# Kernel tuning notes

Hardware: AMD Instinct MI355X
Metric: run time of the kernel (lower is better)

Reference implementation:

```python
import jax, jax.numpy as jnp
import numpy as np

N, E, G = 30000, 240000, 1500
EMB, NODE_DIM, EDGE_DIM, TASKS = 300, 9, 3, 12
L_ENC, L_RAT = 5, 2
GAMMA, T_CON = 0.4, 0.2


def _w(key, shape, fan_in):
    return jax.random.normal(key, shape, jnp.float32) / np.float32(np.sqrt(fan_in))


def setup_inputs() -> dict:
    key = jax.random.key(0)
    ks = jax.random.split(key, 32)
    inp = {}
    inp['x'] = jax.random.normal(ks[0], (N, NODE_DIM), jnp.float32)
    inp['edge_attr'] = jax.random.normal(ks[1], (E, EDGE_DIM), jnp.float32)
    inp['edge_index'] = jax.random.randint(ks[2], (2, E), 0, N, jnp.int32)
    b = jnp.sort(jax.random.randint(ks[3], (N,), 0, G, jnp.int32))
    inp['batch'] = b.at[0].set(0).at[-1].set(G - 1)
    u = jax.random.uniform(ks[4], (N, 2), jnp.float32, 1e-6, 1.0 - 1e-6)
    inp['gumbel'] = -jnp.log(-jnp.log(u))  # standard Gumbel noise (tau=1)
    inp['perm'] = jax.random.permutation(ks[5], G).astype(jnp.int32)
    inp['W_enc'] = _w(ks[6], (NODE_DIM, EMB), NODE_DIM)
    inp['b_enc'] = jnp.zeros((EMB,), jnp.float32)
    inp['We_g'] = _w(ks[7], (L_ENC, EDGE_DIM, EMB), EDGE_DIM)
    inp['be_g'] = jnp.zeros((L_ENC, EMB), jnp.float32)
    inp['W1_g'] = _w(ks[8], (L_ENC, EMB, 2 * EMB), EMB)
    inp['b1_g'] = jnp.zeros((L_ENC, 2 * EMB), jnp.float32)
    inp['W2_g'] = _w(ks[9], (L_ENC, 2 * EMB, EMB), 2 * EMB)
    inp['b2_g'] = jnp.zeros((L_ENC, EMB), jnp.float32)
    inp['We_r'] = _w(ks[10], (L_RAT, EDGE_DIM, EMB), EDGE_DIM)
    inp['be_r'] = jnp.zeros((L_RAT, EMB), jnp.float32)
    inp['W1_r'] = _w(ks[11], (L_RAT, EMB, 2 * EMB), EMB)
    inp['b1_r'] = jnp.zeros((L_RAT, 2 * EMB), jnp.float32)
    inp['W2_r'] = _w(ks[12], (L_RAT, 2 * EMB, EMB), 2 * EMB)
    inp['b2_r'] = jnp.zeros((L_RAT, EMB), jnp.float32)
    inp['Wg1'] = _w(ks[13], (EMB, 2 * EMB), EMB)
    inp['bg1'] = jnp.zeros((2 * EMB,), jnp.float32)
    inp['Wg2'] = _w(ks[14], (2 * EMB, 2), 2 * EMB)
    inp['bg2'] = jnp.zeros((2,), jnp.float32)
    inp['Wp1'] = _w(ks[15], (EMB, 2 * EMB), EMB)
    inp['bp1'] = jnp.zeros((2 * EMB,), jnp.float32)
    inp['Wp2'] = _w(ks[16], (2 * EMB, TASKS), 2 * EMB)
    inp['bp2'] = jnp.zeros((TASKS,), jnp.float32)
    return inp


def _gin_stack(x, src, dst, edge_attr, We, be, W1, b1, W2, b2):
    # GIN-style message passing with edge features, residual, JK='last'.
    L = We.shape[0]
    for l in range(L):
        e = edge_attr @ We[l] + be[l]                               # [E, EMB]
        msg = jax.nn.relu(x[src] + e)                                # gather [E, EMB]
        agg = jax.ops.segment_sum(msg, dst, num_segments=x.shape[0])  # scatter [N, EMB]
        h = jax.nn.relu((agg + x) @ W1[l] + b1[l]) @ W2[l] + b2[l]
        if l < L - 1:
            h = jax.nn.relu(h)
        x = x + h  # residual
    return x


def _mlp2(h, Wa, ba, Wb, bb):
    # Linear -> (BN=identity in eval) -> ReLU -> (Dropout=identity) -> Linear
    return jax.nn.relu(h @ Wa + ba) @ Wb + bb


def _forward(x, edge_attr, gumbel, W_enc, b_enc, We_g, be_g, W1_g, b1_g, W2_g, b2_g,
             We_r, be_r, W1_r, b1_r, W2_r, b2_r, Wg1, bg1, Wg2, bg2, Wp1, bp1, Wp2, bp2,
             edge_index, batch, perm):
    src, dst = edge_index[0], edge_index[1]
    cnt = jnp.clip(jax.ops.segment_sum(jnp.ones((x.shape[0],), jnp.float32), batch, num_segments=G), 1.0)[:, None]

    def gmean(v):
        return jax.ops.segment_sum(v, batch, num_segments=G) / cnt

    x_feat = x @ W_enc + b_enc                                      # node encoder
    h_node = _gin_stack(x_feat, src, dst, edge_attr, We_g, be_g, W1_g, b1_g, W2_g, b2_g)
    x_rat = _gin_stack(x_feat, src, dst, edge_attr, We_r, be_r, W1_r, b1_r, W2_r, b2_r)

    gate_logits = _mlp2(x_rat, Wg1, bg1, Wg2, bg2)                  # [N, 2]
    gate = jax.nn.softmax(gate_logits + gumbel, axis=-1)[:, 1:2]     # gumbel-softmax (soft), keep last col

    h_r = gmean(gate * h_node)
    h_env = gmean((1.0 - gate) * h_node)
    r_num = jax.ops.segment_sum(gate, batch, num_segments=G) + 1e-8
    env_num = jax.ops.segment_sum(1.0 - gate, batch, num_segments=G) + 1e-8

    pred_rem = _mlp2(h_r, Wp1, bp1, Wp2, bp2)
    loss_reg = jnp.abs(r_num / (r_num + env_num) - GAMMA).mean()

    h_out = gmean(h_node)
    na = jnp.linalg.norm(h_r, axis=1)
    nb = jnp.linalg.norm(h_out, axis=1)
    nc = jnp.linalg.norm(h_env, axis=1)
    sim = jnp.exp((h_r @ h_out.T) / (na[:, None] * nb[None, :] + 1e-8) / T_CON)
    sim_cp = jnp.exp((h_r @ h_env.T) / (na[:, None] * nc[None, :] + 1e-8) / T_CON)
    pos = jnp.diagonal(sim)
    loss_con = -jnp.log(pos / (sim_cp.sum(axis=1) + pos)).mean()

    pred_rep = _mlp2(h_r + h_env[perm], Wp1, bp1, Wp2, bp2)
    return pred_rep, pred_rem, loss_reg, loss_con


def reference(x, edge_attr, gumbel, W_enc, b_enc, We_g, be_g, W1_g, b1_g, W2_g, b2_g,
              We_r, be_r, W1_r, b1_r, W2_r, b2_r, Wg1, bg1, Wg2, bg2, Wp1, bp1, Wp2, bp2,
              edge_index, batch, perm):
    return _forward(x, edge_attr, gumbel, W_enc, b_enc, We_g, be_g, W1_g, b1_g, W2_g, b2_g,
                    We_r, be_r, W1_r, b1_r, W2_r, b2_r, Wg1, bg1, Wg2, bg2, Wp1, bp1, Wp2, bp2,
                    edge_index, batch, perm)
```

## Files before the change

kernel.cpp:

```cpp
#include <hip/hip_runtime.h>
#include <hip/hip_bf16.h>

typedef __hip_bfloat16 bf16;
typedef __attribute__((ext_vector_type(8))) short bf16x8;
typedef __attribute__((ext_vector_type(4))) float f32x4;

#define NN 30000
#define NE 240000
#define NG 1500
#define EMB 300
#define HID 600
#define NTASK 12
#define SEM 320
#define SHID 608
#define CG 75
#define NBLK_SCAN 118

__device__ __forceinline__ float tof(bf16 v){ return __bfloat162float(v); }
__device__ __forceinline__ bf16  tob(float v){ return __float2bfloat16(v); }
__device__ __forceinline__ float b2f(unsigned short u){ return __uint_as_float(((unsigned)u)<<16); }

__global__ __launch_bounds__(256) void k_hist(const int* __restrict__ dst, int* __restrict__ deg){
    int e = blockIdx.x*256 + threadIdx.x;
    if (e < NE) atomicAdd(&deg[dst[e]], 1);
// ... 37 lines not shown
        __syncthreads();
        s[t] += add;
        __syncthreads();
    }
    int excl = s[t] - v + boff[b];
    if (i < NN){ indptr[i] = excl; cursor[i] = excl; }
    if (i == 0) indptr[NN] = NE;
}

__global__ __launch_bounds__(256) void k_scatter(const int* __restrict__ dst, int* __restrict__ cursor,
                                                 int* __restrict__ eid){
    int e = blockIdx.x*256 + threadIdx.x;
    if (e < NE){ int p = atomicAdd(&cursor[dst[e]], 1); eid[p] = e; }
}

__global__ __launch_bounds__(256) void k_eprep(const int* __restrict__ eid, const int* __restrict__ src,
                                               const float* __restrict__ eattr, float4* __restrict__ epack){
    int k = blockIdx.x*256 + threadIdx.x;
    if (k >= NE) return;
    int e = eid[k];
    float4 p;
    p.x = __int_as_float(src[e]);
    p.y = eattr[e*3]; p.z = eattr[e*3+1]; p.w = eattr[e*3+2];
    epack[k] = p;
}

__global__ __launch_bounds__(256) void k_wprep_all(
        const float* __restrict__ W1_g, const float* __restrict__ W2_g,
        const float* __restrict__ W1_r, const float* __restrict__ W2_r,
        const float* __restrict__ Wg1,  const float* __restrict__ Wp1,
        bf16* __restrict__ wt1g, bf16* __restrict__ wt2g,
        bf16* __restrict__ wt1r, bf16* __restrict__ wt2r,
        bf16* __restrict__ wtg1, bf16* __restrict__ wtp1,
        int* __restrict__ deg, const int* __restrict__ batch, int* __restrict__ gstart){
    __shared__ float t[32][33];
    int z = blockIdx.z;
    if (z == 16){
        int i = (blockIdx.y*19 + blockIdx.x)*256 + threadIdx.x;
        if (i < NN) deg[i] = 0;
        return;
    }
    if (z == 17){
        int g = (blockIdx.y*19 + blockIdx.x)*256 + threadIdx.x;
        if (g > NG) return;
        if (g == NG){ gstart[NG] = NN; return; }
        int lo=0, hi=NN;
        while (lo<hi){ int mid=(lo+hi)>>1; if (batch[mid] < g) lo=mid+1; else hi=mid; }
        gstart[g] = lo;
        return;
    }
    const float* Ws; bf16* Wd; int K, Kp, N;
    if (z < 5)      { Ws = W1_g + (size_t)z*EMB*HID;      Wd = wt1g + (size_t)z*HID*SEM;      K=EMB; Kp=SEM;  N=HID; }
    else if (z < 10){ int l=z-5;  Ws = W2_g + (size_t)l*HID*EMB; Wd = wt2g + (size_t)l*EMB*SHID; K=HID; Kp=SHID; N=EMB; }
    else if (z < 12){ int l=z-10; Ws = W1_r + (size_t)l*EMB*HID; Wd = wt1r + (size_t)l*HID*SEM;  K=EMB; Kp=SEM;  N=HID; }
    else if (z < 14){ int l=z-12; Ws = W2_r + (size_t)l*HID*EMB; Wd = wt2r + (size_t)l*EMB*SHID; K=HID; Kp=SHID; N=EMB; }
    else if (z ==14){ Ws = Wg1; Wd = wtg1; K=EMB; Kp=SEM; N=HID; }
    else            { Ws = Wp1; Wd = wtp1; K=EMB; Kp=SEM; N=HID; }
    int n0 = blockIdx.x*32, k0 = blockIdx.y*32;
    if (n0 >= N || k0 >= Kp) return;
    int tx = threadIdx.x & 31, ty = threadIdx.x >> 5;
    #pragma unroll
    for (int i=0;i<4;i++){
        int k = k0 + ty + i*8, n = n0 + tx;
        t[ty+i*8][tx] = (k<K && n<N) ? Ws[(size_t)k*N+n] : 0.f;
    }
    __syncthreads();
    #pragma unroll
    for (int i=0;i<4;i++){
        int n = n0 + ty + i*8, k = k0 + tx;
        if (n<N && k<Kp) Wd[(size_t)n*Kp+k] = tob(t[tx][ty+i*8]);
    }
}

__global__ __launch_bounds__(256) void k_encoder(const float* __restrict__ x, const float* __restrict__ W,
                                                 const float* __restrict__ b, bf16* __restrict__ xfeat){
    int idx = blockIdx.x*256 + threadIdx.x;
    if (idx >= NN*EMB) return;
    int n = idx / EMB, c = idx - n*EMB;
    float acc = b[c];
    #pragma unroll
    for (int k=0;k<9;k++) acc += x[n*9+k] * W[k*EMB+c];
    xfeat[(size_t)n*SEM + c] = tob(acc);
}

__device__ __forceinline__ void agg4_body(const bf16* __restrict__ cur, const float* __restrict__ We,
                      const float* __restrict__ be, const float4* __restrict__ epack,
                      const int* __restrict__ indptr, bf16* __restrict__ apx, int idx){
    int n = idx / CG, cg = idx - n*CG;
    int c0 = cg*4;
    float w0[4], w1[4], w2[4], bbv[4], acc[4];
    #pragma unroll
    for (int j=0;j<4;j++){
        w0[j] = We[c0+j]; w1[j] = We[EMB+c0+j]; w2[j] = We[2*EMB+c0+j]; bbv[j] = be[c0+j];
    }
    ushort4 hs = *(const ushort4*)&cur[(size_t)n*SEM + c0];
    acc[0]=b2f(hs.x); acc[1]=b2f(hs.y); acc[2]=b2f(hs.z); acc[3]=b2f(hs.w);
    int k  = indptr[n], k1 = indptr[n+1];

    auto accum4 = [&](float4 e0, float4 e1, float4 e2, float4 e3,
                      ushort4 ha, ushort4 hb, ushort4 hc, ushort4 hd){
        float fa[4] = {b2f(ha.x), b2f(ha.y), b2f(ha.z), b2f(ha.w)};
        float fb[4] = {b2f(hb.x), b2f(hb.y), b2f(hb.z), b2f(hb.w)};
        float fc[4] = {b2f(hc.x), b2f(hc.y), b2f(hc.z), b2f(hc.w)};
        float fd[4] = {b2f(hd.x), b2f(hd.y), b2f(hd.z), b2f(hd.w)};
        #pragma unroll
        for (int j=0;j<4;j++){
            float va = fa[j] + e0.y*w0[j] + e0.z*w1[j] + e0.w*w2[j] + bbv[j];
            float vb = fb[j] + e1.y*w0[j] + e1.z*w1[j] + e1.w*w2[j] + bbv[j];
            float vc = fc[j] + e2.y*w0[j] + e2.z*w1[j] + e2.w*w2[j] + bbv[j];
            float vd = fd[j] + e3.y*w0[j] + e3.z*w1[j] + e3.w*w2[j] + bbv[j];
            acc[j] += fmaxf(va, 0.f) + fmaxf(vb, 0.f) + fmaxf(vc, 0.f) + fmaxf(vd, 0.f);
        }
    };

    if (k + 4 <= k1){
// ... 82 lines not shown
        ushort4 hb = *(const ushort4*)&cur[(size_t)s1*SEM + c0];
        float fa[4] = {b2f(ha.x), b2f(ha.y), b2f(ha.z), b2f(ha.w)};
        float fb[4] = {b2f(hb.x), b2f(hb.y), b2f(hb.z), b2f(hb.w)};
        #pragma unroll
        for (int j=0;j<4;j++){
            accA[j] += fmaxf(fa[j] + e0.y*a0[j] + e0.z*a1[j] + e0.w*a2[j] + ab[j], 0.f)
                     + fmaxf(fb[j] + e1.y*a0[j] + e1.z*a1[j] + e1.w*a2[j] + ab[j], 0.f);
            accB[j] += fmaxf(fa[j] + e0.y*b0[j] + e0.z*b1[j] + e0.w*b2[j] + bb[j], 0.f)
                     + fmaxf(fb[j] + e1.y*b0[j] + e1.z*b1[j] + e1.w*b2[j] + bb[j], 0.f);
        }
    }
    if (k < k1){
        float4 e0 = epack[k];
        int s0 = __float_as_int(e0.x);
        ushort4 ha = *(const ushort4*)&cur[(size_t)s0*SEM + c0];
        float fa[4] = {b2f(ha.x), b2f(ha.y), b2f(ha.z), b2f(ha.w)};
        #pragma unroll
        for (int j=0;j<4;j++){
            accA[j] += fmaxf(fa[j] + e0.y*a0[j] + e0.z*a1[j] + e0.w*a2[j] + ab[j], 0.f);
            accB[j] += fmaxf(fa[j] + e0.y*b0[j] + e0.z*b1[j] + e0.w*b2[j] + bb[j], 0.f);
        }
    }
    ushort4 oA, oB;
    oA.x=__bfloat16_as_ushort(tob(accA[0])); oA.y=__bfloat16_as_ushort(tob(accA[1]));
    oA.z=__bfloat16_as_ushort(tob(accA[2])); oA.w=__bfloat16_as_ushort(tob(accA[3]));
    oB.x=__bfloat16_as_ushort(tob(accB[0])); oB.y=__bfloat16_as_ushort(tob(accB[1]));
    oB.z=__bfloat16_as_ushort(tob(accB[2])); oB.w=__bfloat16_as_ushort(tob(accB[3]));
    *(ushort4*)&apxA[(size_t)n*SEM + c0] = oA;
    *(ushort4*)&apxB[(size_t)n*SEM + c0] = oB;
}

__device__ __forceinline__ void gemm_body(const bf16* __restrict__ A, const bf16* __restrict__ Bt,
        const float* __restrict__ bias, const bf16* __restrict__ R, bf16* __restrict__ C,
        int M, int N, int Kp, int ldc, int relu_out, short* lds){
    short* Ct = lds;
    const int CS = 136;
    int tid = threadIdx.x;
    int wave = tid >> 6, lane = tid & 63;
    int wm = wave >> 1, wn = wave & 1;
    int m0 = blockIdx.y*128, n0 = blockIdx.x*128;

    int srow = tid >> 1;
    int sq   = (tid & 1) * 2;
    int grA = min(m0 + srow, M-1);
    int grB = min(n0 + srow, N-1);
    const bf16* pA = A  + (size_t)grA*Kp + sq*8;
    const bf16* pB = Bt + (size_t)grB*Kp + sq*8;
    int aoff0 = ((srow>>4)*64 +  sq   *16 + (srow&15))*8;
    int aoff1 = ((srow>>4)*64 + (sq+1)*16 + (srow&15))*8;

    f32x4 acc[4][4];
    #pragma unroll
    for (int i=0;i<4;i++){
        #pragma unroll
        for (int j=0;j<4;j++) acc[i][j] = (f32x4){0.f,0.f,0.f,0.f};
    }

    int KC = Kp >> 5;
    uint4 ra0 = *(const uint4*)(pA);
    uint4 ra1 = *(const uint4*)(pA + 8);
    uint4 rb0 = *(const uint4*)(pB);
    uint4 rb1 = *(const uint4*)(pB + 8);
    *(uint4*)(lds + aoff0)        = ra0;
    *(uint4*)(lds + aoff1)        = ra1;
    *(uint4*)(lds + 4096 + aoff0) = rb0;
    *(uint4*)(lds + 4096 + aoff1) = rb1;
    __syncthreads();
    if (KC > 1){
        ra0 = *(const uint4*)(pA + 32); ra1 = *(const uint4*)(pA + 40);
        rb0 = *(const uint4*)(pB + 32); rb1 = *(const uint4*)(pB + 40);
    }

    for (int kc=0; kc<KC; ++kc){
// ... 37 lines not shown
            for (int r=0;r<4;r++){
                float v = acc[i][j][r] + bv;
                if (relu_out) v = fmaxf(v, 0.f);
                Ct[(rl+r)*CS + cl] = (short)__bfloat16_as_ushort(tob(v));
            }
        }
    }
    __syncthreads();
    #pragma unroll
    for (int p=0;p<8;p++){
        int rl = p*16 + (tid>>4);
        int cl = (tid&15)*8;
        int row = m0 + rl, col = n0 + cl;
        if (row < M && col < N){
            union { short s8[8]; uint4 v; } u;
            u.v = *(uint4*)&Ct[rl*CS + cl];
            if (R){
                const bf16* rp = &R[(size_t)row*ldc + col];
                #pragma unroll
                for (int e=0;e<8;e++){
                    float v = b2f((unsigned short)u.s8[e]) + tof(rp[e]);
                    u.s8[e] = (short)__bfloat16_as_ushort(tob(v));
                }
            }
            *(uint4*)&C[(size_t)row*ldc + col] = u.v;
        }
    }
}

__global__ __launch_bounds__(256) void k_gemm2(const bf16* __restrict__ A, const bf16* __restrict__ Bt,
        const float* __restrict__ bias, const bf16* __restrict__ R, bf16* __restrict__ C,
        int M, int N, int Kp, int ldc, int relu_out){
    __shared__ __align__(16) char ldsbuf[34816];
    gemm_body(A, Bt, bias, R, C, M, N, Kp, ldc, relu_out, (short*)ldsbuf);
}

__global__ __launch_bounds__(256) void k_gemm2z(
        const bf16* __restrict__ A0, const bf16* __restrict__ A1,
        const bf16* __restrict__ Bt0, const bf16* __restrict__ Bt1,
        const float* __restrict__ bias0, const float* __restrict__ bias1,
        const bf16* __restrict__ R0, const bf16* __restrict__ R1,
        bf16* __restrict__ C0, bf16* __restrict__ C1,
        int M, int N, int Kp, int ldc, int relu0, int relu1){
    __shared__ __align__(16) char ldsbuf[34816];
    if (blockIdx.z == 0) gemm_body(A0, Bt0, bias0, R0, C0, M, N, Kp, ldc, relu0, (short*)ldsbuf);
    else                 gemm_body(A1, Bt1, bias1, R1, C1, M, N, Kp, ldc, relu1, (short*)ldsbuf);
}

__device__ __forceinline__ void stage_tile(const short* __restrict__ P, int RB, int K, int r0, int k0,
                                           short (*lds)[64][8], int tid){
    #pragma unroll
    for (int s=0;s<2;s++){
        int seg = tid*2+s;
        int row = seg>>2, q = seg&3;
        int gr = r0 + row;
        int gk = k0 + q*8;
        union { short s8[8]; uint4 v; } u;
        if (gr < RB && gk + 8 <= K){
            const uint2* p = (const uint2*)(P + (size_t)gr*K + gk);
            uint2 lo = p[0], hi = p[1];
            u.v.x = lo.x; u.v.y = lo.y; u.v.z = hi.x; u.v.w = hi.y;
        } else {
            #pragma unroll
            for (int j=0;j<8;j++){
                int kk = gk + j;
                u.s8[j] = (gr < RB && kk < K) ? P[(size_t)gr*K + kk] : (short)0;
            }
        }
        *(uint4*)&lds[row>>4][q*16 + (row&15)][0] = u.v;
    }
}

__device__ __forceinline__ void sim_body(const bf16* __restrict__ A, const bf16* __restrict__ Bt,
                      const float* __restrict__ na, const float* __restrict__ nc, float* __restrict__ C,
                      char* ldsraw){
    short (*Asl)[64][8] = (short(*)[64][8])ldsraw;
    short (*Bsl)[64][8] = (short(*)[64][8])(ldsraw + 8192);
    int tid = threadIdx.x;
    int wave = tid >> 6, lane = tid & 63;
    int wm = wave >> 1, wn = wave & 1;
    int m0 = blockIdx.y*128, n0 = blockIdx.x*128;
    f32x4 acc[4][4];
    #pragma unroll
    for (int i=0;i<4;i++){
        #pragma unroll
        for (int j=0;j<4;j++) acc[i][j] = (f32x4){0.f,0.f,0.f,0.f};
    }
    for (int k0=0; k0<SEM; k0+=32){
        stage_tile((const short*)A,  NG, SEM, m0, k0, Asl, tid);
        stage_tile((const short*)Bt, NG, SEM, n0, k0, Bsl, tid);
        __syncthreads();
        bf16x8 af[4], bfr[4];
        #pragma unroll
        for (int i=0;i<4;i++) af[i]  = *(const bf16x8*)&Asl[wm*4+i][lane][0];
        #pragma unroll
        for (int j=0;j<4;j++) bfr[j] = *(const bf16x8*)&Bsl[wn*4+j][lane][0];
        #pragma unroll
        for (int i=0;i<4;i++){
            #pragma unroll
            for (int j=0;j<4;j++)
                acc[i][j] = __builtin_amdgcn_mfma_f32_16x16x32_bf16(af[i], bfr[j], acc[i][j], 0, 0, 0);
        }
        __syncthreads();
    }
    int lq = lane >> 4, lr = lane & 15;
    #pragma unroll
    for (int i=0;i<4;i++){
        int rb = m0 + (wm*4+i)*16 + lq*4;
        #pragma unroll
        for (int j=0;j<4;j++){
            int col = n0 + (wn*4+j)*16 + lr;
            if (col >= NG) continue;
            float ncj = nc[col];
            #pragma unroll
            for (int r=0;r<4;r++){
                int row = rb + r;
                if (row >= NG) continue;
                C[(size_t)row*NG+col] = expf(acc[i][j][r] * 5.0f / (na[row]*ncj + 1e-8f));
            }
        }
    }
}

__global__ __launch_bounds__(256) void k_simhead(const bf16* __restrict__ hrb, const bf16* __restrict__ henvb,
        const float* __restrict__ na, const float* __restrict__ nc, float* __restrict__ simcp,
        const bf16* __restrict__ Pbuf, const bf16* __restrict__ wtp1, const float* __restrict__ bp1,
        bf16* __restrict__ hidP){
    __shared__ __align__(16) char ldsbuf[34816];
    if (blockIdx.z == 0){
        if (blockIdx.x >= 12 || blockIdx.y >= 12) return;
        sim_body(hrb, henvb, na, nc, simcp, ldsbuf);
    } else {
        if (blockIdx.x >= 5) return;
        gemm_body(Pbuf, wtp1, bp1, nullptr, hidP, 2*NG, HID, SEM, SHID, 1, (short*)ldsbuf);
    }
}

__global__ __launch_bounds__(256) void k_gate(const bf16* __restrict__ mid, const float* __restrict__ Wg2,
                      const float* __restrict__ bg2, const float* __restrict__ gumbel, float* __restrict__ gate){
    int gw = blockIdx.x*4 + (threadIdx.x >> 6);
    int lane = threadIdx.x & 63;
    if (gw >= NN) return;
    float s0=0.f, s1=0.f;
    for (int i=lane;i<HID;i+=64){
        float h = tof(mid[(size_t)gw*SHID+i]);
        s0 += h * Wg2[i*2];
        s1 += h * Wg2[i*2+1];
    }
    for (int off=32; off>0; off>>=1){ s0 += __shfl_down(s0, off); s1 += __shfl_down(s1, off); }
    if (lane==0){
        float l0 = s0 + bg2[0] + gumbel[gw*2];
        float l1 = s1 + bg2[1] + gumbel[gw*2+1];
        float m = fmaxf(l0,l1);
        float e0 = expf(l0-m), e1 = expf(l1-m);
        gate[gw] = e1/(e0+e1);
    }
}

__global__ __launch_bounds__(320) void k_pool(const bf16* __restrict__ h, const float* __restrict__ gate,
                      const int* __restrict__ gstart, float* __restrict__ sumh, float* __restrict__ sumgh,
                      float* __restrict__ rnum, float* __restrict__ cntf){
    int g = blockIdx.x, c = threadIdx.x;
    if (c >= EMB) return;
    int n0 = gstart[g], n1 = gstart[g+1];
    float sh=0.f, sg=0.f, sgate=0.f;
    for (int n=n0;n<n1;n++){
        float v = tof(h[(size_t)n*SEM+c]);
        float gt = gate[n];
        sh += v; sg += gt*v;
        if (c==0) sgate += gt;
    }
    sumh[g*EMB+c] = sh; sumgh[g*EMB+c] = sg;
    if (c==0){ rnum[g] = sgate; cntf[g] = (float)(n1-n0); }
}

__global__ __launch_bounds__(320) void k_meannorm(const float* __restrict__ sumh, const float* __restrict__ sumgh,
                      const float* __restrict__ cntf, float* __restrict__ hr, float* __restrict__ henv,
                      float* __restrict__ hout, bf16* __restrict__ hrb, bf16* __restrict__ henvb,
                      bf16* __restrict__ P, float* __restrict__ na, float* __restrict__ nc,
                      float* __restrict__ pos){
    int g = blockIdx.x, c = threadIdx.x;
    float r=0.f, e=0.f, o=0.f;
    int idx = g*SEM + c;
    if (c < EMB){
        int off = g*EMB + c;
        float inv = 1.f / fmaxf(cntf[g], 1.f);
        float sh = sumh[off], sg = sumgh[off];
        r = sg*inv; e = (sh-sg)*inv; o = sh*inv;
        hr[off] = r; henv[off] = e; hout[off] = o;
        hrb[idx] = tob(r); henvb[idx] = tob(e); P[idx] = tob(r);
    } else {
        hrb[idx] = tob(0.f); henvb[idx] = tob(0.f); P[idx] = tob(0.f);
    }
    float srr=r*r, soo=o*o, see=e*e, sro=r*o;
    #pragma unroll
    for (int off=32; off>0; off>>=1){
        srr += __shfl_down(srr,off); soo += __shfl_down(soo,off);
        see += __shfl_down(see,off); sro += __shfl_down(sro,off);
    }
    __shared__ float ws[4][5];
    int wv = c >> 6, ln = c & 63;
    if (ln == 0){ ws[0][wv]=srr; ws[1][wv]=soo; ws[2][wv]=see; ws[3][wv]=sro; }
    __syncthreads();
    if (c == 0){
        float a=0.f,b=0.f,c2=0.f,d=0.f;
        #pragma unroll
        for (int i=0;i<5;i++){ a+=ws[0][i]; b+=ws[1][i]; c2+=ws[2][i]; d+=ws[3][i]; }
        float sa = sqrtf(a), sb = sqrtf(b), sc = sqrtf(c2);
        na[g] = sa; nc[g] = sc;
        pos[g] = expf(d/(sa*sb + 1e-8f) * 5.0f);
    }
}

__global__ __launch_bounds__(256) void k_pbuild2(const float* __restrict__ hr, const float* __restrict__ henv,
                      const int* __restrict__ perm, bf16* __restrict__ P){
    int idx = blockIdx.x*256 + threadIdx.x;
    if (idx >= NG*SEM) return;
    int g = idx / SEM, c = idx - g*SEM;
    P[(size_t)(NG+g)*SEM + c] = (c < EMB)
        ? tob(hr[g*EMB+c] + henv[(size_t)perm[g]*EMB + c])
        : tob(0.f);
}

__global__ __launch_bounds__(256) void k_rowsum(const float* __restrict__ simcp, float* __restrict__ S){
    __shared__ float red[256];
    int g = blockIdx.x, t = threadIdx.x;
    float s = 0.f;
    for (int j=t;j<NG;j+=256) s += simcp[(size_t)g*NG+j];
    red[t]=s; __syncthreads();
    for (int off=128; off>0; off>>=1){ if (t<off) red[t]+=red[t+off]; __syncthreads(); }
    if (t==0) S[g]=red[0];
}

__global__ __launch_bounds__(256) void k_pred(const bf16* __restrict__ hidP, const float* __restrict__ Wp2,
                      const float* __restrict__ bp2, float* __restrict__ out){
    int r = blockIdx.x*4 + (threadIdx.x >> 6);
    int lane = threadIdx.x & 63;
    if (r >= 2*NG) return;
    float acc[NTASK];
    #pragma unroll
    for (int t=0;t<NTASK;t++) acc[t] = 0.f;
    for (int i=lane;i<HID;i+=64){
        float h = tof(hidP[(size_t)r*SHID+i]);
        const float4* wp = (const float4*)&Wp2[i*NTASK];
        float4 wa = wp[0], wb = wp[1], wc = wp[2];
        acc[0]+=h*wa.x; acc[1]+=h*wa.y; acc[2]+=h*wa.z; acc[3]+=h*wa.w;
        acc[4]+=h*wb.x; acc[5]+=h*wb.y; acc[6]+=h*wb.z; acc[7]+=h*wb.w;
        acc[8]+=h*wc.x; acc[9]+=h*wc.y; acc[10]+=h*wc.z; acc[11]+=h*wc.w;
    }
    #pragma unroll
    for (int t=0;t<NTASK;t++){
        for (int off=32; off>0; off>>=1) acc[t] += __shfl_down(acc[t], off);
    }
    if (lane==0){
        float* dst = (r < NG) ? &out[NG*NTASK + r*NTASK] : &out[(r-NG)*NTASK];
        #pragma unroll
        for (int t=0;t<NTASK;t++) dst[t] = acc[t] + bp2[t];
    }
}

__global__ __launch_bounds__(256) void k_loss(const float* __restrict__ cntf, const float* __restrict__ rnum,
                      const float* __restrict__ pos, const float* __restrict__ S, float* __restrict__ out){
    __shared__ float ra[256], rb[256];
    int t = threadIdx.x;
// ... 29 lines not shown
    const float* W1_g   = (const float*)d_in[10];
    const float* b1_g   = (const float*)d_in[11];
    const float* W2_g   = (const float*)d_in[12];
    const float* b2_g   = (const float*)d_in[13];
    const float* We_r   = (const float*)d_in[14];
    const float* be_r   = (const float*)d_in[15];
    const float* W1_r   = (const float*)d_in[16];
    const float* b1_r   = (const float*)d_in[17];
    const float* W2_r   = (const float*)d_in[18];
    const float* b2_r   = (const float*)d_in[19];
    const float* Wg1    = (const float*)d_in[20];
    const float* bg1    = (const float*)d_in[21];
    const float* Wg2    = (const float*)d_in[22];
    const float* bg2    = (const float*)d_in[23];
    const float* Wp1    = (const float*)d_in[24];
    const float* bp1    = (const float*)d_in[25];
    const float* Wp2    = (const float*)d_in[26];
    const float* bp2    = (const float*)d_in[27];
    float* out = (float*)d_out;

    const int* srcArr = eidx;
    const int* dstArr = eidx + NE;

    char* w = (char*)d_ws;
    size_t off = 0;
    auto alloc = [&](size_t bytes)->char*{ char* p = w + off; off += (bytes + 255) & ~(size_t)255; return p; };
    bf16* xfeat = (bf16*)alloc((size_t)NN*SEM*2);
    bf16* cur_r = (bf16*)alloc((size_t)NN*SEM*2);
    bf16* cur_g = (bf16*)alloc((size_t)NN*SEM*2);
    bf16* apx   = (bf16*)alloc((size_t)NN*SEM*2);
    bf16* apx2  = (bf16*)alloc((size_t)NN*SEM*2);
    char* midc  = alloc((size_t)NN*SHID*2);
    bf16* mid_r = (bf16*)midc;
    float* simcp = (float*)midc;
    bf16* Pbuf   = (bf16*)(midc + 12*1024*1024);
    bf16* hidP   = (bf16*)(midc + 20*1024*1024);
    bf16* mid_g = (bf16*)alloc((size_t)NN*SHID*2);
    bf16* wt1g  = (bf16*)alloc((size_t)5*HID*SEM*2);
    bf16* wt2g  = (bf16*)alloc((size_t)5*EMB*SHID*2);
    bf16* wt1r  = (bf16*)alloc((size_t)2*HID*SEM*2);
    bf16* wt2r  = (bf16*)alloc((size_t)2*EMB*SHID*2);
    bf16* wtg1  = (bf16*)alloc((size_t)HID*SEM*2);
    bf16* wtp1  = (bf16*)alloc((size_t)HID*SEM*2);
    float4* epack = (float4*)alloc((size_t)NE*16);
    float* gate  = (float*)alloc((size_t)NN*4);
    float* sumh  = (float*)alloc((size_t)NG*EMB*4);
    float* sumgh = (float*)alloc((size_t)NG*EMB*4);
    float* hr    = (float*)alloc((size_t)NG*EMB*4);
    float* henv  = (float*)alloc((size_t)NG*EMB*4);
    float* hout  = (float*)alloc((size_t)NG*EMB*4);
    bf16* hrb    = (bf16*)alloc((size_t)NG*SEM*2);
    bf16* henvb  = (bf16*)alloc((size_t)NG*SEM*2);
    float* rnum  = (float*)alloc(NG*4);
    float* cntf  = (float*)alloc(NG*4);
    float* na    = (float*)alloc(NG*4);
    float* ncv   = (float*)alloc(NG*4);
    float* pos   = (float*)alloc(NG*4);
    float* Ssum  = (float*)alloc(NG*4);
    int* deg     = (int*)alloc((size_t)NN*4);
    int* indptr  = (int*)alloc((size_t)(NN+1)*4);
    int* cursor  = (int*)alloc((size_t)NN*4);
    int* eid     = (int*)alloc((size_t)NE*4);
    int* gstart  = (int*)alloc((size_t)(NG+1)*4);
    int* bsum    = (int*)alloc((size_t)NBLK_SCAN*4);
    int* boff    = (int*)alloc((size_t)NBLK_SCAN*4);

    const int NB_NE  = (NE+255)/256;
    const int NB_NC  = (NN*EMB+255)/256;
    const int NB_AG  = (NN*CG+255)/256;
    const int NB_GP  = (NG*SEM+255)/256;

    dim3 gwp(19, 19, 18);
    k_wprep_all<<<gwp, 256, 0, stream>>>(W1_g, W2_g, W1_r, W2_r, Wg1, Wp1,
                                         wt1g, wt2g, wt1r, wt2r, wtg1, wtp1,
                                         deg, batch, gstart);

    k_hist   <<<NB_NE, 256, 0, stream>>>(dstArr, deg);
    k_scanA  <<<NBLK_SCAN, 256, 0, stream>>>(deg, bsum);
    k_scanB  <<<1, 128, 0, stream>>>(bsum, boff);
    k_scanC  <<<NBLK_SCAN, 256, 0, stream>>>(deg, boff, indptr, cursor);
    k_scatter<<<NB_NE, 256, 0, stream>>>(dstArr, cursor, eid);
    k_eprep  <<<NB_NE, 256, 0, stream>>>(eid, srcArr, eattr, epack);

    dim3 gm1z((HID+127)/128, (NN+127)/128, 2);
    dim3 gm2z((EMB+127)/128, (NN+127)/128, 2);
    dim3 gm1((HID+127)/128, (NN+127)/128);
    dim3 gm2((EMB+127)/128, (NN+127)/128);
    dim3 gagz(NB_AG, 1, 2);

    k_encoder<<<NB_NC, 256, 0, stream>>>(x, W_enc, b_enc, xfeat);

    k_agg4d<<<NB_AG, 256, 0, stream>>>(xfeat, We_r, be_r, We_g, be_g, epack, indptr, apx, apx2);
    k_gemm2z<<<gm1z, 256, 0, stream>>>(apx, apx2, wt1r, wt1g, b1_r, b1_g,
                                       nullptr, nullptr, mid_r, mid_g, NN, HID, SEM, SHID, 1, 1);
    k_gemm2z<<<gm2z, 256, 0, stream>>>(mid_r, mid_g, wt2r, wt2g, b2_r, b2_g,
                                       xfeat, xfeat, cur_r, cur_g, NN, EMB, SHID, SEM, 1, 1);

    k_agg4z<<<gagz, 256, 0, stream>>>(cur_r, cur_g, We_r + 3*EMB, We_g + 3*EMB, be_r + EMB, be_g + EMB,
                                      epack, indptr, apx, apx2);
    k_gemm2z<<<gm1z, 256, 0, stream>>>(apx, apx2, wt1r + (size_t)HID*SEM, wt1g + (size_t)HID*SEM,
                                       b1_r + HID, b1_g + HID, nullptr, nullptr, mid_r, mid_g,
                                       NN, HID, SEM, SHID, 1, 1);
    k_gemm2z<<<gm2z, 256, 0, stream>>>(mid_r, mid_g, wt2r + (size_t)EMB*SHID, wt2g + (size_t)EMB*SHID,
                                       b2_r + EMB, b2_g + EMB, cur_r, cur_g, cur_r, cur_g,
                                       NN, EMB, SHID, SEM, 0, 1);

    k_agg4 <<<NB_AG, 256, 0, stream>>>(cur_g, We_g + 2*3*EMB, be_g + 2*EMB, epack, indptr, apx2);
    k_gemm2z<<<gm1z, 256, 0, stream>>>(cur_r, apx2, wtg1, wt1g + (size_t)2*HID*SEM,
                                       bg1, b1_g + 2*HID, nullptr, nullptr, mid_r, mid_g,
                                       NN, HID, SEM, SHID, 1, 1);
    k_gemm2<<<gm2, 256, 0, stream>>>(mid_g, wt2g + (size_t)2*EMB*SHID, b2_g + 2*EMB, cur_g, cur_g,
                                     NN, EMB, SHID, SEM, 1);
    k_gate<<<NN/4, 256, 0, stream>>>(mid_r, Wg2, bg2, gumbel, gate);

    for (int l=3; l<5; l++){
        k_agg4 <<<NB_AG, 256, 0, stream>>>(cur_g, We_g + l*3*EMB, be_g + l*EMB, epack, indptr, apx2);
        k_gemm2<<<gm1, 256, 0, stream>>>(apx2, wt1g + (size_t)l*HID*SEM, b1_g + l*HID, nullptr, mid_g,
                                         NN, HID, SEM, SHID, 1);
        k_gemm2<<<gm2, 256, 0, stream>>>(mid_g, wt2g + (size_t)l*EMB*SHID, b2_g + l*EMB, cur_g, cur_g,
                                         NN, EMB, SHID, SEM, (l<4)?1:0);
    }

    k_pool    <<<NG, 320, 0, stream>>>(cur_g, gate, gstart, sumh, sumgh, rnum, cntf);
    k_meannorm<<<NG, 320, 0, stream>>>(sumh, sumgh, cntf, hr, henv, hout, hrb, henvb, Pbuf, na, ncv, pos);
    k_pbuild2 <<<NB_GP, 256, 0, stream>>>(hr, henv, perm, Pbuf);
    dim3 gsh(12, 24, 2);
    k_simhead<<<gsh, 256, 0, stream>>>(hrb, henvb, na, ncv, simcp, Pbuf, wtp1, bp1, hidP);
    k_rowsum<<<NG, 256, 0, stream>>>(simcp, Ssum);
    k_pred  <<<(2*NG+3)/4, 256, 0, stream>>>(hidP, Wp2, bp2, out);
    k_loss  <<<1, 256, 0, stream>>>(cntf, rnum, pos, Ssum, out);
}
```

Baseline: 963.0 us.

## Fuse gate head into GEMM epilogue, use 128x64 tiles, fold encoder and rowsum

Several changes land together. The encoder is folded into the weight-prep launch, and the gate's second layer is computed inside the first gate GEMM epilogue using shuffle reductions and atomics, so the mid_r activations are no longer re-read. The gate GEMM is also co-scheduled with the GNN layer's first GEMM in a single launch. The N=300 GEMMs switch to 128x64 tiles to cut padded-column waste, and the similarity row sums are reduced in the sim kernel's epilogue instead of writing a 1500x1500 matrix and summing it in a separate pass. The cost is float atomics, which make summation order nondeterministic, and extra zero-initialisation.

Result: slower. 1.005 ms (+4.3%).

```diff
diff --git a/kernel.cpp b/kernel.cpp
--- a/kernel.cpp
+++ b/kernel.cpp
@@ -93,12 +93,25 @@
         bf16* __restrict__ wt1g, bf16* __restrict__ wt2g,
         bf16* __restrict__ wt1r, bf16* __restrict__ wt2r,
         bf16* __restrict__ wtg1, bf16* __restrict__ wtp1,
-        int* __restrict__ deg, const int* __restrict__ batch, int* __restrict__ gstart){
+        int* __restrict__ deg, const int* __restrict__ batch, int* __restrict__ gstart,
+        const float* __restrict__ x, const float* __restrict__ W_enc,
+        const float* __restrict__ b_enc, bf16* __restrict__ xfeat,
+        float* __restrict__ glogit){
     __shared__ float t[32][33];
     int z = blockIdx.z;
+    if (z >= 18){
+        int idx = ((z-18)*361 + blockIdx.y*19 + blockIdx.x)*256 + threadIdx.x;
+        if (idx >= NN*EMB) return;
+        int n = idx / EMB, c = idx - n*EMB;
+        float acc = b_enc[c];
+        #pragma unroll
+        for (int k=0;k<9;k++) acc += x[n*9+k] * W_enc[k*EMB+c];
+        xfeat[(size_t)n*SEM + c] = tob(acc);
+        return;
+    }
     if (z == 16){
         int i = (blockIdx.y*19 + blockIdx.x)*256 + threadIdx.x;
-        if (i < NN) deg[i] = 0;
+        if (i < NN){ deg[i] = 0; glogit[2*i] = 0.f; glogit[2*i+1] = 0.f; }
         return;
     }
     if (z == 17){
@@ -131,17 +144,6 @@
         int n = n0 + ty + i*8, k = k0 + tx;
         if (n<N && k<Kp) Wd[(size_t)n*Kp+k] = tob(t[tx][ty+i*8]);
     }
-}
-
-__global__ __launch_bounds__(256) void k_encoder(const float* __restrict__ x, const float* __restrict__ W,
-                                                 const float* __restrict__ b, bf16* __restrict__ xfeat){
-    int idx = blockIdx.x*256 + threadIdx.x;
-    if (idx >= NN*EMB) return;
-    int n = idx / EMB, c = idx - n*EMB;
-    float acc = b[c];
-    #pragma unroll
-    for (int k=0;k<9;k++) acc += x[n*9+k] * W[k*EMB+c];
-    xfeat[(size_t)n*SEM + c] = tob(acc);
 }
 
 __device__ __forceinline__ void agg4_body(const bf16* __restrict__ cur, const float* __restrict__ We,
@@ -290,13 +292,12 @@
 
 __device__ __forceinline__ void gemm_body(const bf16* __restrict__ A, const bf16* __restrict__ Bt,
         const float* __restrict__ bias, const bf16* __restrict__ R, bf16* __restrict__ C,
-        int M, int N, int Kp, int ldc, int relu_out, short* lds){
+        int M, int N, int Kp, int ldc, int relu_out, short* lds, int m0, int n0){
     short* Ct = lds;
     const int CS = 136;
     int tid = threadIdx.x;
     int wave = tid >> 6, lane = tid & 63;
     int wm = wave >> 1, wn = wave & 1;
-    int m0 = blockIdx.y*128, n0 = blockIdx.x*128;
 
     int srow = tid >> 1;
     int sq   = (tid & 1) * 2;
@@ -400,7 +401,8 @@
         const float* __restrict__ bias, const bf16* __restrict__ R, bf16* __restrict__ C,
         int M, int N, int Kp, int ldc, int relu_out){
     __shared__ __align__(16) char ldsbuf[34816];
-    gemm_body(A, Bt, bias, R, C, M, N, Kp, ldc, relu_out, (short*)ldsbuf);
+    gemm_body(A, Bt, bias, R, C, M, N, Kp, ldc, relu_out, (short*)ldsbuf,
+              blockIdx.y*128, blockIdx.x*128);
 }
 
 __global__ __launch_bounds__(256) void k_gemm2z(
@@ -411,8 +413,256 @@
         bf16* __restrict__ C0, bf16* __restrict__ C1,
         int M, int N, int Kp, int ldc, int relu0, int relu1){
     __shared__ __align__(16) char ldsbuf[34816];
-    if (blockIdx.z == 0) gemm_body(A0, Bt0, bias0, R0, C0, M, N, Kp, ldc, relu0, (short*)ldsbuf);
-    else                 gemm_body(A1, Bt1, bias1, R1, C1, M, N, Kp, ldc, relu1, (short*)ldsbuf);
+    int m0 = blockIdx.y*128, n0 = blockIdx.x*128;
+    if (blockIdx.z == 0) gemm_body(A0, Bt0, bias0, R0, C0, M, N, Kp, ldc, relu0, (short*)ldsbuf, m0, n0);
+    else                 gemm_body(A1, Bt1, bias1, R1, C1, M, N, Kp, ldc, relu1, (short*)ldsbuf, m0, n0);
+}
+
+__device__ __forceinline__ void gemm64_body(const bf16* __restrict__ A, const bf16* __restrict__ Bt,
+        const float* __restrict__ bias, const bf16* __restrict__ R, bf16* __restrict__ C,
+        int M, int N, int Kp, int ldc, int relu_out, short* lds, int m0, int n0){
+    short* Ct = lds;
+    const int CS = 72;
+    int tid = threadIdx.x;
+    int wave = tid >> 6, lane = tid & 63;
+    int wm = wave >> 1, wn = wave & 1;
+
+    int srow = tid >> 1;
+    int sq   = (tid & 1) * 2;
+    int grA = min(m0 + srow, M-1);
+    const bf16* pA = A + (size_t)grA*Kp + sq*8;
+    int aoff0 = ((srow>>4)*64 +  sq   *16 + (srow&15))*8;
+    int aoff1 = ((srow>>4)*64 + (sq+1)*16 + (srow&15))*8;
+
+    int brow = tid >> 2;
+    int bq   = tid & 3;
+    int grB = min(n0 + brow, N-1);
+    const bf16* pB = Bt + (size_t)grB*Kp + bq*8;
+    int boff = ((brow>>4)*64 + bq*16 + (brow&15))*8;
+
+    f32x4 acc[4][2];
+    #pragma unroll
+    for (int i=0;i<4;i++){
+        #pragma unroll
+        for (int j=0;j<2;j++) acc[i][j] = (f32x4){0.f,0.f,0.f,0.f};
+    }
+
+    int KC = Kp >> 5;
+    uint4 ra0 = *(const uint4*)(pA);
+    uint4 ra1 = *(const uint4*)(pA + 8);
+    uint4 rb0 = *(const uint4*)(pB);
+    *(uint4*)(lds + aoff0)       = ra0;
+    *(uint4*)(lds + aoff1)       = ra1;
+    *(uint4*)(lds + 4096 + boff) = rb0;
+    __syncthreads();
+    if (KC > 1){
+        ra0 = *(const uint4*)(pA + 32); ra1 = *(const uint4*)(pA + 40);
+        rb0 = *(const uint4*)(pB + 32);
+    }
+
+    for (int kc=0; kc<KC; ++kc){
+        short* cbuf = lds + (kc & 1)*6144;
+        short* nbuf = lds + ((kc+1) & 1)*6144;
+        if (kc+1 < KC){
+            *(uint4*)(nbuf + aoff0)       = ra0;
+            *(uint4*)(nbuf + aoff1)       = ra1;
+            *(uint4*)(nbuf + 4096 + boff) = rb0;
+            if (kc+2 < KC){
+                const bf16* qA = pA + (kc+2)*32;
+                ra0 = *(const uint4*)(qA); ra1 = *(const uint4*)(qA+8);
+                rb0 = *(const uint4*)(pB + (kc+2)*32);
+            }
+        }
+        bf16x8 af[4], bfr[2];
+        #pragma unroll
+        for (int i=0;i<4;i++) af[i]  = *(const bf16x8*)(cbuf + ((wm*4+i)*64 + lane)*8);
+        #pragma unroll
+        for (int j=0;j<2;j++) bfr[j] = *(const bf16x8*)(cbuf + 4096 + ((wn*2+j)*64 + lane)*8);
+        #pragma unroll
+        for (int i=0;i<4;i++){
+            #pragma unroll
+            for (int j=0;j<2;j++)
+                acc[i][j] = __builtin_amdgcn_mfma_f32_16x16x32_bf16(af[i], bfr[j], acc[i][j], 0, 0, 0);
+        }
+        __syncthreads();
+    }
+
+    int lq = lane >> 4, lr = lane & 15;
+    #pragma unroll
+    for (int i=0;i<4;i++){
+        int rl = (wm*4+i)*16 + lq*4;
+        #pragma unroll
+        for (int j=0;j<2;j++){
+            int cl = (wn*2+j)*16 + lr;
+            float bv = bias[min(n0+cl, N-1)];
+            #pragma unroll
+            for (int r=0;r<4;r++){
+                float v = acc[i][j][r] + bv;
+                if (relu_out) v = fmaxf(v, 0.f);
+                Ct[(rl+r)*CS + cl] = (short)__bfloat16_as_ushort(tob(v));
+            }
+        }
+    }
+    __syncthreads();
+    #pragma unroll
+    for (int p=0;p<4;p++){
+        int rl = p*32 + (tid>>3);
+        int cl = (tid&7)*8;
+        int row = m0 + rl, col = n0 + cl;
+        if (row < M && col < N){
+            union { short s8[8]; uint4 v; } u;
+            u.v = *(uint4*)&Ct[rl*CS + cl];
+            if (R){
+                const bf16* rp = &R[(size_t)row*ldc + col];
+                #pragma unroll
+                for (int e=0;e<8;e++){
+                    float v = b2f((unsigned short)u.s8[e]) + tof(rp[e]);
+                    u.s8[e] = (short)__bfloat16_as_ushort(tob(v));
+                }
+            }
+            *(uint4*)&C[(size_t)row*ldc + col] = u.v;
+        }
+    }
+}
+
+__global__ __launch_bounds__(256) void k_gemm64(const bf16* __restrict__ A, const bf16* __restrict__ Bt,
+        const float* __restrict__ bias, const bf16* __restrict__ R, bf16* __restrict__ C,
+        int M, int N, int Kp, int ldc, int relu_out){
+    __shared__ __align__(16) char ldsbuf[24576];
+    gemm64_body(A, Bt, bias, R, C, M, N, Kp, ldc, relu_out, (short*)ldsbuf,
+                blockIdx.y*128, blockIdx.x*64);
+}
+
+__global__ __launch_bounds__(256) void k_gemm64z(
+        const bf16* __restrict__ A0, const bf16* __restrict__ A1,
+        const bf16* __restrict__ Bt0, const bf16* __restrict__ Bt1,
+        const float* __restrict__ bias0, const float* __restrict__ bias1,
+        const bf16* __restrict__ R0, const bf16* __restrict__ R1,
+        bf16* __restrict__ C0, bf16* __restrict__ C1,
+        int M, int N, int Kp, int ldc, int relu0, int relu1){
+    __shared__ __align__(16) char ldsbuf[24576];
+    int m0 = blockIdx.y*128, n0 = blockIdx.x*64;
+    if (blockIdx.z == 0) gemm64_body(A0, Bt0, bias0, R0, C0, M, N, Kp, ldc, relu0, (short*)ldsbuf, m0, n0);
+    else                 gemm64_body(A1, Bt1, bias1, R1, C1, M, N, Kp, ldc, relu1, (short*)ldsbuf, m0, n0);
+}
+
+__device__ __forceinline__ void gate_gemm_body(const bf16* __restrict__ A, const bf16* __restrict__ Bt,
+        const float* __restrict__ bias, const float* __restrict__ Wg2, float* __restrict__ glogit,
+        int M, int N, int Kp, short* lds, int m0, int n0){
+    int tid = threadIdx.x;
+    int wave = tid >> 6, lane = tid & 63;
+    int wm = wave >> 1, wn = wave & 1;
+
+    int srow = tid >> 1;
+    int sq   = (tid & 1) * 2;
+    int grA = min(m0 + srow, M-1);
+    int grB = min(n0 + srow, N-1);
+    const bf16* pA = A  + (size_t)grA*Kp + sq*8;
+    const bf16* pB = Bt + (size_t)grB*Kp + sq*8;
+    int aoff0 = ((srow>>4)*64 +  sq   *16 + (srow&15))*8;
+    int aoff1 = ((srow>>4)*64 + (sq+1)*16 + (srow&15))*8;
+
+    f32x4 acc[4][4];
+    #pragma unroll
+    for (int i=0;i<4;i++){
+        #pragma unroll
+        for (int j=0;j<4;j++) acc[i][j] = (f32x4){0.f,0.f,0.f,0.f};
+    }
+
+    int KC = Kp >> 5;
+    uint4 ra0 = *(const uint4*)(pA);
+    uint4 ra1 = *(const uint4*)(pA + 8);
+    uint4 rb0 = *(const uint4*)(pB);
+    uint4 rb1 = *(const uint4*)(pB + 8);
+    *(uint4*)(lds + aoff0)        = ra0;
+    *(uint4*)(lds + aoff1)        = ra1;
+    *(uint4*)(lds + 4096 + aoff0) = rb0;
+    *(uint4*)(lds + 4096 + aoff1) = rb1;
+    __syncthreads();
+    if (KC > 1){
+        ra0 = *(const uint4*)(pA + 32); ra1 = *(const uint4*)(pA + 40);
+        rb0 = *(const uint4*)(pB + 32); rb1 = *(const uint4*)(pB + 40);
+    }
+
+    for (int kc=0; kc<KC; ++kc){
+        short* cbuf = lds + (kc & 1)*8192;
+        short* nbuf = lds + ((kc+1) & 1)*8192;
+        if (kc+1 < KC){
+            *(uint4*)(nbuf + aoff0)        = ra0;
+            *(uint4*)(nbuf + aoff1)        = ra1;
+            *(uint4*)(nbuf + 4096 + aoff0) = rb0;
+            *(uint4*)(nbuf + 4096 + aoff1) = rb1;
+            if (kc+2 < KC){
+                const bf16* qA = pA + (kc+2)*32;
+                const bf16* qB = pB + (kc+2)*32;
+                ra0 = *(const uint4*)(qA); ra1 = *(const uint4*)(qA+8);
+                rb0 = *(const uint4*)(qB); rb1 = *(const uint4*)(qB+8);
+            }
+        }
+        bf16x8 af[4], bfr[4];
+        #pragma unroll
+        for (int i=0;i<4;i++) af[i]  = *(const bf16x8*)(cbuf + ((wm*4+i)*64 + lane)*8);
+        #pragma unroll
+        for (int j=0;j<4;j++) bfr[j] = *(const bf16x8*)(cbuf + 4096 + ((wn*4+j)*64 + lane)*8);
+        #pragma unroll
+        for (int i=0;i<4;i++){
+            #pragma unroll
+            for (int j=0;j<4;j++)
+                acc[i][j] = __builtin_amdgcn_mfma_f32_16x16x32_bf16(af[i], bfr[j], acc[i][j], 0, 0, 0);
+        }
+        __syncthreads();
+    }
+
+    int lq = lane >> 4, lr = lane & 15;
+    #pragma unroll
+    for (int i=0;i<4;i++){
+        #pragma unroll
+        for (int r=0;r<4;r++){
+            int row = m0 + (wm*4+i)*16 + lq*4 + r;
+            float p0 = 0.f, p1 = 0.f;
+            #pragma unroll
+            for (int j=0;j<4;j++){
+                int cl = (wn*4+j)*16 + lr;
+                int col = n0 + cl;
+                float v = fmaxf(acc[i][j][r] + bias[min(col, N-1)], 0.f);
+                if (col < N){ p0 += v * Wg2[col*2]; p1 += v * Wg2[col*2+1]; }
+            }
+            #pragma unroll
+            for (int m=1; m<16; m<<=1){ p0 += __shfl_xor(p0, m); p1 += __shfl_xor(p1, m); }
+            if (lr == 0 && row < M){
+                atomicAdd(&glogit[row*2],   p0);
+                atomicAdd(&glogit[row*2+1], p1);
+            }
+        }
+    }
+}
+
+__global__ __launch_bounds__(256) void k_gatepair(
+        const bf16* __restrict__ Ag, const bf16* __restrict__ Btg, const float* __restrict__ bg,
+        const float* __restrict__ Wg2, float* __restrict__ glogit,
+        const bf16* __restrict__ A1, const bf16* __restrict__ Bt1, const float* __restrict__ b1,
+        bf16* __restrict__ C1){
+    __shared__ __align__(16) char ldsbuf[34816];
+    int bid = blockIdx.x;
+    if (bid < 1175){
+        gate_gemm_body(Ag, Btg, bg, Wg2, glogit, NN, HID, SEM, (short*)ldsbuf,
+                       (bid/5)*128, (bid%5)*128);
+    } else {
+        int gb = bid - 1175;
+        gemm_body(A1, Bt1, b1, nullptr, C1, NN, HID, SEM, SHID, 1, (short*)ldsbuf,
+                  (gb/5)*128, (gb%5)*128);
+    }
+}
+
+__global__ __launch_bounds__(256) void k_gatefin(const float* __restrict__ glogit,
+        const float* __restrict__ bg2, const float* __restrict__ gumbel, float* __restrict__ gate){
+    int i = blockIdx.x*256 + threadIdx.x;
+    if (i >= NN) return;
+    float l0 = glogit[2*i]   + bg2[0] + gumbel[2*i];
+    float l1 = glogit[2*i+1] + bg2[1] + gumbel[2*i+1];
+    float m = fmaxf(l0, l1);
+    float e0 = expf(l0-m), e1 = expf(l1-m);
+    gate[i] = e1/(e0+e1);
 }
 
 __device__ __forceinline__ void stage_tile(const short* __restrict__ P, int RB, int K, int r0, int k0,
@@ -440,7 +690,7 @@
 }
 
 __device__ __forceinline__ void sim_body(const bf16* __restrict__ A, const bf16* __restrict__ Bt,
-                      const float* __restrict__ na, const float* __restrict__ nc, float* __restrict__ C,
+                      const float* __restrict__ na, const float* __restrict__ nc, float* __restrict__ S,
                       char* ldsraw){
     short (*Asl)[64][8] = (short(*)[64][8])ldsraw;
     short (*Bsl)[64][8] = (short(*)[64][8])(ldsraw + 8192);
@@ -474,54 +724,37 @@
     int lq = lane >> 4, lr = lane & 15;
     #pragma unroll
     for (int i=0;i<4;i++){
-        int rb = m0 + (wm*4+i)*16 + lq*4;
-        #pragma unroll
-        for (int j=0;j<4;j++){
-            int col = n0 + (wn*4+j)*16 + lr;
-            if (col >= NG) continue;
-            float ncj = nc[col];
+        #pragma unroll
+        for (int r=0;r<4;r++){
+            int row = m0 + (wm*4+i)*16 + lq*4 + r;
+            float nar = na[min(row, NG-1)];
+            float rsum = 0.f;
             #pragma unroll
-            for (int r=0;r<4;r++){
-                int row = rb + r;
-                if (row >= NG) continue;
-                C[(size_t)row*NG+col] = expf(acc[i][j][r] * 5.0f / (na[row]*ncj + 1e-8f));
+            for (int j=0;j<4;j++){
+                int col = n0 + (wn*4+j)*16 + lr;
+                float ncj = nc[min(col, NG-1)];
+                float e = expf(acc[i][j][r] * 5.0f / (nar*ncj + 1e-8f));
+                if (row < NG && col < NG) rsum += e;
             }
+            #pragma unroll
+            for (int m=1; m<16; m<<=1) rsum += __shfl_xor(rsum, m);
+            if (lr == 0 && row < NG) atomicAdd(&S[row], rsum);
         }
     }
 }
 
 __global__ __launch_bounds__(256) void k_simhead(const bf16* __restrict__ hrb, const bf16* __restrict__ henvb,
-        const float* __restrict__ na, const float* __restrict__ nc, float* __restrict__ simcp,
+        const float* __restrict__ na, const float* __restrict__ nc, float* __restrict__ Ssum,
         const bf16* __restrict__ Pbuf, const bf16* __restrict__ wtp1, const float* __restrict__ bp1,
         bf16* __restrict__ hidP){
     __shared__ __align__(16) char ldsbuf[34816];
     if (blockIdx.z == 0){
         if (blockIdx.x >= 12 || blockIdx.y >= 12) return;
-        sim_body(hrb, henvb, na, nc, simcp, ldsbuf);
+        sim_body(hrb, henvb, na, nc, Ssum, ldsbuf);
     } else {
         if (blockIdx.x >= 5) return;
-        gemm_body(Pbuf, wtp1, bp1, nullptr, hidP, 2*NG, HID, SEM, SHID, 1, (short*)ldsbuf);
-    }
-}
-
-__global__ __launch_bounds__(256) void k_gate(const bf16* __restrict__ mid, const float* __restrict__ Wg2,
-                      const float* __restrict__ bg2, const float* __restrict__ gumbel, float* __restrict__ gate){
-    int gw = blockIdx.x*4 + (threadIdx.x >> 6);
-    int lane = threadIdx.x & 63;
-    if (gw >= NN) return;
-    float s0=0.f, s1=0.f;
-    for (int i=lane;i<HID;i+=64){
-        float h = tof(mid[(size_t)gw*SHID+i]);
-        s0 += h * Wg2[i*2];
-        s1 += h * Wg2[i*2+1];
-    }
-    for (int off=32; off>0; off>>=1){ s0 += __shfl_down(s0, off); s1 += __shfl_down(s1, off); }
-    if (lane==0){
-        float l0 = s0 + bg2[0] + gumbel[gw*2];
-        float l1 = s1 + bg2[1] + gumbel[gw*2+1];
-        float m = fmaxf(l0,l1);
-        float e0 = expf(l0-m), e1 = expf(l1-m);
-        gate[gw] = e1/(e0+e1);
+        gemm_body(Pbuf, wtp1, bp1, nullptr, hidP, 2*NG, HID, SEM, SHID, 1, (short*)ldsbuf,
+                  blockIdx.y*128, blockIdx.x*128);
     }
 }
 
@@ -546,7 +779,7 @@
                       const float* __restrict__ cntf, float* __restrict__ hr, float* __restrict__ henv,
                       float* __restrict__ hout, bf16* __restrict__ hrb, bf16* __restrict__ henvb,
                       bf16* __restrict__ P, float* __restrict__ na, float* __restrict__ nc,
-                      float* __restrict__ pos){
+                      float* __restrict__ pos, float* __restrict__ Ssum){
     int g = blockIdx.x, c = threadIdx.x;
     float r=0.f, e=0.f, o=0.f;
     int idx = g*SEM + c;
@@ -559,6 +792,7 @@
         hrb[idx] = tob(r); henvb[idx] = tob(e); P[idx] = tob(r);
     } else {
         hrb[idx] = tob(0.f); henvb[idx] = tob(0.f); P[idx] = tob(0.f);
+        if (c == 319) Ssum[g] = 0.f;
     }
     float srr=r*r, soo=o*o, see=e*e, sro=r*o;
     #pragma unroll
@@ -588,16 +822,6 @@
     P[(size_t)(NG+g)*SEM + c] = (c < EMB)
         ? tob(hr[g*EMB+c] + henv[(size_t)perm[g]*EMB + c])
         : tob(0.f);
-}
-
-__global__ __launch_bounds__(256) void k_rowsum(const float* __restrict__ simcp, float* __restrict__ S){
-    __shared__ float red[256];
-    int g = blockIdx.x, t = threadIdx.x;
-    float s = 0.f;
-    for (int j=t;j<NG;j+=256) s += simcp[(size_t)g*NG+j];
-    red[t]=s; __syncthreads();
-    for (int off=128; off>0; off>>=1){ if (t<off) red[t]+=red[t+off]; __syncthreads(); }
-    if (t==0) S[g]=red[0];
 }
 
 __global__ __launch_bounds__(256) void k_pred(const bf16* __restrict__ hidP, const float* __restrict__ Wp2,
@@ -693,7 +917,6 @@
     bf16* apx2  = (bf16*)alloc((size_t)NN*SEM*2);
     char* midc  = alloc((size_t)NN*SHID*2);
     bf16* mid_r = (bf16*)midc;
-    float* simcp = (float*)midc;
     bf16* Pbuf   = (bf16*)(midc + 12*1024*1024);
     bf16* hidP   = (bf16*)(midc + 20*1024*1024);
     bf16* mid_g = (bf16*)alloc((size_t)NN*SHID*2);
@@ -705,6 +928,7 @@
     bf16* wtp1  = (bf16*)alloc((size_t)HID*SEM*2);
     float4* epack = (float4*)alloc((size_t)NE*16);
     float* gate  = (float*)alloc((size_t)NN*4);
+    float* glogit= (float*)alloc((size_t)NN*2*4);
     float* sumh  = (float*)alloc((size_t)NG*EMB*4);
     float* sumgh = (float*)alloc((size_t)NG*EMB*4);
     float* hr    = (float*)alloc((size_t)NG*EMB*4);
@@ -727,14 +951,13 @@
     int* boff    = (int*)alloc((size_t)NBLK_SCAN*4);
 
     const int NB_NE  = (NE+255)/256;
-    const int NB_NC  = (NN*EMB+255)/256;
     const int NB_AG  = (NN*CG+255)/256;
     const int NB_GP  = (NG*SEM+255)/256;
 
-    dim3 gwp(19, 19, 18);
+    dim3 gwp(19, 19, 18 + 98);
     k_wprep_all<<<gwp, 256, 0, stream>>>(W1_g, W2_g, W1_r, W2_r, Wg1, Wp1,
                                          wt1g, wt2g, wt1r, wt2r, wtg1, wtp1,
-                                         deg, batch, gstart);
+                                         deg, batch, gstart, x, W_enc, b_enc, xfeat, glogit);
 
     k_hist   <<<NB_NE, 256, 0, stream>>>(dstArr, deg);
     k_scanA  <<<NBLK_SCAN, 256, 0, stream>>>(deg, bsum);
@@ -744,50 +967,47 @@
     k_eprep  <<<NB_NE, 256, 0, stream>>>(eid, srcArr, eattr, epack);
 
     dim3 gm1z((HID+127)/128, (NN+127)/128, 2);
-    dim3 gm2z((EMB+127)/128, (NN+127)/128, 2);
+    dim3 gm64z((EMB+63)/64, (NN+127)/128, 2);
     dim3 gm1((HID+127)/128, (NN+127)/128);
-    dim3 gm2((EMB+127)/128, (NN+127)/128);
+    dim3 gm64((EMB+63)/64, (NN+127)/128);
     dim3 gagz(NB_AG, 1, 2);
-
-    k_encoder<<<NB_NC, 256, 0, stream>>>(x, W_enc, b_enc, xfeat);
 
     k_agg4d<<<NB_AG, 256, 0, stream>>>(xfeat, We_r, be_r, We_g, be_g, epack, indptr, apx, apx2);
     k_gemm2z<<<gm1z, 256, 0, stream>>>(apx, apx2, wt1r, wt1g, b1_r, b1_g,
                                        nullptr, nullptr, mid_r, mid_g, NN, HID, SEM, SHID, 1, 1);
-    k_gemm2z<<<gm2z, 256, 0, stream>>>(mid_r, mid_g, wt2r, wt2g, b2_r, b2_g,
-                                       xfeat, xfeat, cur_r, cur_g, NN, EMB, SHID, SEM, 1, 1);
+    k_gemm64z<<<gm64z, 256, 0, stream>>>(mid_r, mid_g, wt2r, wt2g, b2_r, b2_g,
+                                         xfeat, xfeat, cur_r, cur_g, NN, EMB, SHID, SEM, 1, 1);
 
     k_agg4z<<<gagz, 256, 0, stream>>>(cur_r, cur_g, We_r + 3*EMB, We_g + 3*EMB, be_r + EMB, be_g + EMB,
                                       epack, indptr, apx, apx2);
     k_gemm2z<<<gm1z, 256, 0, stream>>>(apx, apx2, wt1r + (size_t)HID*SEM, wt1g + (size_t)HID*SEM,
                                        b1_r + HID, b1_g + HID, nullptr, nullptr, mid_r, mid_g,
                                        NN, HID, SEM, SHID, 1, 1);
-    k_gemm2z<<<gm2z, 256, 0, stream>>>(mid_r, mid_g, wt2r + (size_t)EMB*SHID, wt2g + (size_t)EMB*SHID,
-                                       b2_r + EMB, b2_g + EMB, cur_r, cur_g, cur_r, cur_g,
-                                       NN, EMB, SHID, SEM, 0, 1);
+    k_gemm64z<<<gm64z, 256, 0, stream>>>(mid_r, mid_g, wt2r + (size_t)EMB*SHID, wt2g + (size_t)EMB*SHID,
+                                         b2_r + EMB, b2_g + EMB, cur_r, cur_g, cur_r, cur_g,
+                                         NN, EMB, SHID, SEM, 0, 1);
 
     k_agg4 <<<NB_AG, 256, 0, stream>>>(cur_g, We_g + 2*3*EMB, be_g + 2*EMB, epack, indptr, apx2);
-    k_gemm2z<<<gm1z, 256, 0, stream>>>(cur_r, apx2, wtg1, wt1g + (size_t)2*HID*SEM,
-                                       bg1, b1_g + 2*HID, nullptr, nullptr, mid_r, mid_g,
-                                       NN, HID, SEM, SHID, 1, 1);
-    k_gemm2<<<gm2, 256, 0, stream>>>(mid_g, wt2g + (size_t)2*EMB*SHID, b2_g + 2*EMB, cur_g, cur_g,
-                                     NN, EMB, SHID, SEM, 1);
-    k_gate<<<NN/4, 256, 0, stream>>>(mid_r, Wg2, bg2, gumbel, gate);
+    k_gatepair<<<2350, 256, 0, stream>>>(cur_r, wtg1, bg1, Wg2, glogit,
+                                         apx2, wt1g + (size_t)2*HID*SEM, b1_g + 2*HID, mid_g);
+    k_gatefin<<<(NN+255)/256, 256, 0, stream>>>(glogit, bg2, gumbel, gate);
+    k_gemm64<<<gm64, 256, 0, stream>>>(mid_g, wt2g + (size_t)2*EMB*SHID, b2_g + 2*EMB, cur_g, cur_g,
+                                       NN, EMB, SHID, SEM, 1);
 
     for (int l=3; l<5; l++){
         k_agg4 <<<NB_AG, 256, 0, stream>>>(cur_g, We_g + l*3*EMB, be_g + l*EMB, epack, indptr, apx2);
         k_gemm2<<<gm1, 256, 0, stream>>>(apx2, wt1g + (size_t)l*HID*SEM, b1_g + l*HID, nullptr, mid_g,
                                          NN, HID, SEM, SHID, 1);
-        k_gemm2<<<gm2, 256, 0, stream>>>(mid_g, wt2g + (size_t)l*EMB*SHID, b2_g + l*EMB, cur_g, cur_g,
-                                         NN, EMB, SHID, SEM, (l<4)?1:0);
+        k_gemm64<<<gm64, 256, 0, stream>>>(mid_g, wt2g + (size_t)l*EMB*SHID, b2_g + l*EMB, cur_g, cur_g,
+                                           NN, EMB, SHID, SEM, (l<4)?1:0);
     }
 
     k_pool    <<<NG, 320, 0, stream>>>(cur_g, gate, gstart, sumh, sumgh, rnum, cntf);
-    k_meannorm<<<NG, 320, 0, stream>>>(sumh, sumgh, cntf, hr, henv, hout, hrb, henvb, Pbuf, na, ncv, pos);
+    k_meannorm<<<NG, 320, 0, stream>>>(sumh, sumgh, cntf, hr, henv, hout, hrb, henvb, Pbuf,
+                                       na, ncv, pos, Ssum);
     k_pbuild2 <<<NB_GP, 256, 0, stream>>>(hr, henv, perm, Pbuf);
     dim3 gsh(12, 24, 2);
-    k_simhead<<<gsh, 256, 0, stream>>>(hrb, henvb, na, ncv, simcp, Pbuf, wtp1, bp1, hidP);
-    k_rowsum<<<NG, 256, 0, stream>>>(simcp, Ssum);
+    k_simhead<<<gsh, 256, 0, stream>>>(hrb, henvb, na, ncv, Ssum, Pbuf, wtp1, bp1, hidP);
     k_pred  <<<(2*NG+3)/4, 256, 0, stream>>>(hidP, Wp2, bp2, out);
     k_loss  <<<1, 256, 0, stream>>>(cntf, rnum, pos, Ssum, out);
 }
```
